# Performance work log

Measured on AMD Instinct MI355X. Metric: run time of the kernel, lower is better.

## Reference

```python
import jax, jax.numpy as jnp
import numpy as np

B, L, E, H, ENC, V, NL = 64, 512, 128, 512, 256, 4, 2
SOS = 4


def setup_inputs() -> dict:
    key = jax.random.key(0)
    ks = jax.random.split(key, 20)
    s = 0.05
    r = lambda k, shp: (jax.random.normal(k, shp, jnp.float32) * s)
    return {
        "encoder_outputs": jax.random.normal(ks[0], (B, L, ENC), jnp.float32),
        "targets": jax.random.randint(ks[1], (B, L), 0, V),
        "encoder_mask": jnp.ones((B, L), bool),
        "teacher_forcing_ratio": 1,
        "emb": r(ks[2], (V + 2, E)),
        "Wh": r(ks[3], (H, H)),
        "Ws": r(ks[4], (H, ENC)),
        "v": r(ks[5], (1, H)),
        "Wih0": r(ks[6], (3 * H, E + ENC)),
        "Whh0": r(ks[7], (3 * H, H)),
        "bih0": r(ks[8], (3 * H,)),
        "bhh0": r(ks[9], (3 * H,)),
        "Wih1": r(ks[10], (3 * H, H)),
        "Whh1": r(ks[11], (3 * H, H)),
        "bih1": r(ks[12], (3 * H,)),
        "bhh1": r(ks[13], (3 * H,)),
        "Wout": r(ks[14], (V, H)),
        "bout": r(ks[15], (V,)),
        "Winit": r(ks[16], (H * NL, ENC)),
        "binit": r(ks[17], (H * NL,)),
    }


def gru_cell(x, h, Wih, Whh, bih, bhh):
    # PyTorch GRUCell math
    gi = x @ Wih.T + bih
    gh = h @ Whh.T + bhh
    ir, iz, inn = jnp.split(gi, 3, axis=-1)
    hr, hz, hn = jnp.split(gh, 3, axis=-1)
    rg = jax.nn.sigmoid(ir + hr)
    zg = jax.nn.sigmoid(iz + hz)
    ng = jnp.tanh(inn + rg * hn)
    return (1.0 - zg) * ng + zg * h


def reference(encoder_outputs, targets, encoder_mask, teacher_forcing_ratio,
              emb, Wh, Ws, v, Wih0, Whh0, bih0, bhh0, Wih1, Whh1, bih1, bhh1,
              Wout, bout, Winit, binit):
    # init hidden: masked mean-pool -> linear -> tanh, (NL, B, H)
    maskf = encoder_mask[..., None].astype(jnp.float32)
    pooled = (encoder_outputs * maskf).sum(1) / jnp.clip(maskf.sum(1), 1.0)
    h0 = jnp.tanh((pooled @ Winit.T + binit).reshape(B, NL, H).transpose(1, 0, 2))

    # attention keys precomputed once (same linear applied each step in torch)
    keys = jnp.einsum('ble,he->blh', encoder_outputs, Ws)  # (B, L, H)

    # teacher forcing ratio fixed at 1 -> inputs known ahead of time
    tokens = jnp.concatenate([jnp.full((B, 1), SOS, targets.dtype), targets[:, :-1]], axis=1)
    emb_seq = emb[tokens]  # (B, L, E)

    neg = jnp.finfo(jnp.float32).min

    def step(h, e_t):
        q = h[-1] @ Wh.T                                   # (B, H)
        energy = jnp.tanh(q[:, None, :] + keys)            # (B, L, H)
        scores = jnp.einsum('blh,h->bl', energy, v[0])     # (B, L)
        scores = jnp.where(encoder_mask, scores, neg)
        attn = jax.nn.softmax(scores, axis=-1)
        ctx = jnp.einsum('bl,ble->be', attn, encoder_outputs)
        x = jnp.concatenate([e_t, ctx], axis=-1)           # (B, E+ENC)
        h0n = gru_cell(x, h[0], Wih0, Whh0, bih0, bhh0)
        h1n = gru_cell(h0n, h[1], Wih1, Whh1, bih1, bhh1)
        logits = h1n @ Wout.T + bout                       # (B, V)
        return jnp.stack([h0n, h1n]), logits

    _, logits = jax.lax.scan(step, h0, emb_seq.transpose(1, 0, 2))
    return logits.transpose(1, 0, 2)  # (B, L, V)
```

## Files before the change

### kernel.cpp

```cpp
#include <hip/hip_runtime.h>
#include <cstdint>
#include <cstddef>


#define BB   64
#define LL   512
#define EE   128
#define HH   512
#define ED   256
#define VV   4
#define SOS  4

#define NBLK 512
#define NTHR 256

typedef unsigned short ushort8 __attribute__((ext_vector_type(8)));
typedef unsigned int uint;
typedef uint  uint4v  __attribute__((ext_vector_type(4)));
typedef float float4v __attribute__((ext_vector_type(4)));

static const size_t OFF_KEYS = 0;
static const size_t OFF_WH   = 33554432;
static const size_t OFF_WHH0 = 34078720;
static const size_t OFF_WIH1 = 35651584;
static const size_t OFF_WHH1 = 37224448;
static const size_t OFF_WIHC = 38797312;
static const size_t OFF_GTOK = 39583744;
static const size_t OFF_H0   = 39620608;
static const size_t OFF_H1   = 39751680;
static const size_t OFF_QQ   = 39882752;
static const size_t OFF_CTXP = 40407040;
static const size_t OFF_SS   = 40931328;
static const size_t OFF_H0Q  = 40933376;
static const size_t OFF_H1Q  = 40998912;
static const size_t OFF_FLG  = 41064448;
static const size_t OFF_CNT  = 41097216;
static const size_t OFF_LP   = 41097728;

#define L_KEYS 0
#define L_H0F  65536
#define L_H1F  66560
#define L_QB   67584
#define L_VV   69696
#define L_CTX  71808
#define L_SCB  72832
#define L_ATB  73088
#define L_RED  73344
#define L_PRED 73408
#define L_GH0  77504
#define L_GH1  78272
#define L_H0O  79040
#define L_H1O  79296
#define L_TOT  79552

#define UC_LD4(dst, ptr) \
  asm volatile("global_load_dwordx4 %0, %1, off sc0 sc1" : "=v"(dst) : "v"(ptr))
#define UC_ST4(ptr, v4) \
  asm volatile("global_store_dwordx4 %0, %1, off sc0 sc1" :: "v"(ptr), "v"(v4) : "memory")
#define UC_FENCE() \
  do { asm volatile("s_waitcnt vmcnt(0)" ::: "memory"); \
       __builtin_amdgcn_sched_barrier(0); } while (0)

__device__ __forceinline__ float bfu(unsigned short u) {
  return __uint_as_float(((unsigned)u) << 16);
}
__device__ __forceinline__ float bflo(uint u) { return __uint_as_float(u << 16); }
__device__ __forceinline__ float bfhi(uint u) { return __uint_as_float(u & 0xffff0000u); }
__device__ __forceinline__ unsigned short f2bf(float f) {
  unsigned u = __float_as_uint(f);
  unsigned r = 0x7FFFu + ((u >> 16) & 1u);
  return (unsigned short)((u + r) >> 16);
}
__device__ __forceinline__ uint packbf(float a, float b) {
  return (uint)f2bf(a) | ((uint)f2bf(b) << 16);
}
__device__ __forceinline__ float tanh_fast(float x) {
  x = __builtin_amdgcn_fmed3f(x, -10.f, 10.f);
  float t = __builtin_amdgcn_exp2f(x * 2.8853900817779268f);
  return (t - 1.f) * __builtin_amdgcn_rcpf(t + 1.f);
}
__device__ __forceinline__ float sigmoid_fast(float x) {
  x = __builtin_amdgcn_fmed3f(x, -30.f, 30.f);
  float t = __builtin_amdgcn_exp2f(x * -1.4426950408889634f);
  return __builtin_amdgcn_rcpf(1.f + t);
}
__device__ __forceinline__ float exp_fast(float x) {
  return __builtin_amdgcn_exp2f(x * 1.4426950408889634f);
}
__device__ __forceinline__ float gloadf(const float* p) {
  return __hip_atomic_load(p, __ATOMIC_RELAXED, __HIP_MEMORY_SCOPE_AGENT);
}
__device__ __forceinline__ void gstoref(float* p, float v) {
  __hip_atomic_store(p, v, __ATOMIC_RELAXED, __HIP_MEMORY_SCOPE_AGENT);
}
__device__ __forceinline__ uint gloadu(const uint* p) {
  return __hip_atomic_load(p, __ATOMIC_RELAXED, __HIP_MEMORY_SCOPE_AGENT);
}
__device__ __forceinline__ void gstoreu(uint* p, uint v) {
  __hip_atomic_store(p, v, __ATOMIC_RELAXED, __HIP_MEMORY_SCOPE_AGENT);
}

__device__ __forceinline__ void octet_sync(char* ws, int b, int j, uint gen) {
  asm volatile("s_waitcnt vmcnt(0)" ::: "memory");
  __syncthreads();
  const int tid = threadIdx.x;
  uint* fl = (uint*)(ws + OFF_FLG);
  if (tid == 0)
    gstoreu(fl + (size_t)(b * 8 + j) * 16, gen);
  if (tid < 8 && tid != j) {
    while (gloadu(fl + (size_t)(b * 8 + tid) * 16) < gen)
      __builtin_amdgcn_s_sleep(4);
  }
  __syncthreads();
}


__global__ void k_prep(const float* Wh, const float* Whh0, const float* Wih0,
                       const float* Wih1, const float* Whh1, char* ws) {
  unsigned short* Whbf   = (unsigned short*)(ws + OFF_WH);
  unsigned short* Whh0bf = (unsigned short*)(ws + OFF_WHH0);
  unsigned short* Wih1bf = (unsigned short*)(ws + OFF_WIH1);
  unsigned short* Whh1bf = (unsigned short*)(ws + OFF_WHH1);
  unsigned short* WihCbf = (unsigned short*)(ws + OFF_WIHC);
  const int tot = 262144 + 786432 * 3 + 393216;
  for (int i = blockIdx.x * blockDim.x + threadIdx.x; i < tot; i += gridDim.x * blockDim.x) {
    if (i < 262144) { Whbf[i] = f2bf(Wh[i]); }
    else if (i < 262144 + 786432) { int jj = i - 262144; Whh0bf[jj] = f2bf(Whh0[jj]); }
    else if (i < 262144 + 2 * 786432) { int jj = i - 262144 - 786432; Wih1bf[jj] = f2bf(Wih1[jj]); }
    else if (i < 262144 + 3 * 786432) { int jj = i - 262144 - 2 * 786432; Whh1bf[jj] = f2bf(Whh1[jj]); }
    else {
      int jj = i - 262144 - 3 * 786432;
      int r = jj >> 8, e = jj & 255;
      WihCbf[jj] = f2bf(Wih0[(size_t)r * 384 + 128 + e]);
    }
  }
}

__global__ void k_gitok(const float* emb, const float* Wih0, const float* bih0, char* ws) {
  float* gt = (float*)(ws + OFF_GTOK);
  const int vt = blockIdx.x;
  const int tid = threadIdx.x;
  __shared__ float ev[EE];
  if (tid < EE) ev[tid] = emb[(size_t)vt * EE + tid];
  __syncthreads();
  for (int r = tid; r < 1536; r += 256) {
    float a = bih0[r];
    const float* wr = Wih0 + (size_t)r * 384;
    for (int e = 0; e < EE; ++e) a += wr[e] * ev[e];
    gt[(size_t)vt * 1536 + r] = a;
  }
}

__global__ void k_keys(const float* enc, const float* Ws, char* ws) {
  unsigned short* keys = (unsigned short*)(ws + OFF_KEYS);
  __shared__ float et[32][ED];
  const int tid = threadIdx.x;
  const int row0 = blockIdx.x * 32;
  for (int r = 0; r < 32; ++r) et[r][tid] = enc[(size_t)(row0 + r) * ED + tid];
  __syncthreads();
  for (int hhh = 0; hhh < 2; ++hhh) {
    const int h = hhh * 256 + tid;
    float acc[32];
    #pragma unroll
    for (int ll = 0; ll < 32; ++ll) acc[ll] = 0.f;
    const float4* wrow = (const float4*)(Ws + (size_t)h * ED);
    for (int e4 = 0; e4 < 64; ++e4) {
      float4 w = wrow[e4];
      #pragma unroll
      for (int ll = 0; ll < 32; ++ll) {
        acc[ll] += w.x * et[ll][e4 * 4] + w.y * et[ll][e4 * 4 + 1]
                 + w.z * et[ll][e4 * 4 + 2] + w.w * et[ll][e4 * 4 + 3];
      }
    }
    for (int ll = 0; ll < 32; ++ll)
      keys[(size_t)(row0 + ll) * HH + h] = f2bf(acc[ll]);
  }
}

__global__ void k_init(const float* enc, const float* Winit, const float* binit, char* ws) {
  const int b = blockIdx.x;
  const int tid = threadIdx.x;
  __shared__ float pooled[ED];
  float acc = 0.f;
  for (int l = 0; l < LL; ++l) acc += enc[((size_t)b * LL + l) * ED + tid];
  pooled[tid] = acc * (1.0f / 512.0f);
  __syncthreads();
  float* h0 = (float*)(ws + OFF_H0);
  float* h1 = (float*)(ws + OFF_H1);
  for (int pass = 0; pass < 4; ++pass) {
    const int jj = pass * 256 + tid;
    float a = binit[jj];
    const float* wr = Winit + (size_t)jj * ED;
    for (int e = 0; e < ED; ++e) a += wr[e] * pooled[e];
    const float val = tanh_fast(a);
    const int nl = jj >> 9, h = jj & 511;
    if (nl == 0) h0[(size_t)b * HH + h] = val;
    else h1[(size_t)b * HH + h] = val;
  }
  if (b == 0) {
    uint* fl = (uint*)(ws + OFF_FLG);
    for (int i = tid; i < 8192; i += 256) fl[i] = 0u;
    uint* cnt = (uint*)(ws + OFF_CNT);
    if (tid < 128) cnt[tid] = 0u;
  }
}

__launch_bounds__(NTHR, 2)
__global__ void k_decode(char* ws, const float* enc, const int* targets,
                         const float* vvec, const float* bhh0, const float* bhh1,
                         const float* bih1, const float* Wout) {
  extern __shared__ char smem[];
  const int tid = threadIdx.x;

  __shared__ int roleSh[2];
  if (tid == 0) {
    uint xcd;
    asm volatile("s_getreg_b32 %0, hwreg(HW_REG_XCC_ID)" : "=s"(xcd));
    xcd &= 7u;
    uint* cnt = (uint*)(ws + OFF_CNT);
    uint rank = __hip_atomic_fetch_add(cnt + (size_t)xcd * 16, 1u,
                                       __ATOMIC_RELAXED, __HIP_MEMORY_SCOPE_AGENT);
    roleSh[0] = (int)(rank & 63);
    roleSh[1] = (int)xcd;
  }
  __syncthreads();
  const int b = roleSh[0], j = roleSh[1];

  const unsigned short* keysg  = (const unsigned short*)(ws + OFF_KEYS);
  const unsigned short* Whbf   = (const unsigned short*)(ws + OFF_WH);
  const unsigned short* Whh0bf = (const unsigned short*)(ws + OFF_WHH0);
  const unsigned short* Wih1bf = (const unsigned short*)(ws + OFF_WIH1);
  const unsigned short* Whh1bf = (const unsigned short*)(ws + OFF_WHH1);
  const unsigned short* WihCbf = (const unsigned short*)(ws + OFF_WIHC);
  const float* gi_tok = (const float*)(ws + OFF_GTOK);

  uint*  QQg   = (uint*)(ws + OFF_QQ)   + (size_t)b * 2048;
  float* CTXPg = (float*)(ws + OFF_CTXP) + (size_t)b * 2048;
  float* SSg   = (float*)(ws + OFF_SS)  + (size_t)b * 8;
  uint*  H0Qg  = (uint*)(ws + OFF_H0Q)  + (size_t)b * 256;
  uint*  H1Qg  = (uint*)(ws + OFF_H1Q)  + (size_t)b * 256;
  float* lp    = (float*)(ws + OFF_LP);

  uint*  h0u   = (uint*)(smem + L_H0F);
  uint*  h1u   = (uint*)(smem + L_H1F);
  float* qbf   = (float*)(smem + L_QB);
  float* vvf   = (float*)(smem + L_VV);
  float* ctx   = (float*)(smem + L_CTX);
  float* scb   = (float*)(smem + L_SCB);
  float* atb   = (float*)(smem + L_ATB);
  float* wred  = (float*)(smem + L_RED);
  float* pRed  = (float*)(smem + L_PRED);
  float* gh0own = (float*)(smem + L_GH0);
  float* gh1own = (float*)(smem + L_GH1);
  float* h0own = (float*)(smem + L_H0O);
  float* h1own = (float*)(smem + L_H1O);
  uint*  qstage = (uint*)(smem + L_PRED);
  uint*  hstage = (uint*)(smem + L_SCB);

  for (int c = tid; c < 4096; c += NTHR) {
    const int l = c >> 6, hs = c & 63;
    ushort8 kv = *(const ushort8*)(keysg + ((size_t)(b * LL + j * 64 + l) * HH + hs * 8));
    *(ushort8*)(smem + L_KEYS + l * 1024 + ((hs * 16) ^ ((l & 7) << 4))) = kv;
  }
  for (int h = tid; h < 512; h += NTHR)
    vvf[(h >> 7) * 132 + (h & 127)] = vvec[h];
  {
    const float* H0g = (const float*)(ws + OFF_H0) + (size_t)b * HH;
    const float* H1g = (const float*)(ws + OFF_H1) + (size_t)b * HH;
    h0u[tid] = packbf(H0g[2 * tid], H0g[2 * tid + 1]);
    h1u[tid] = packbf(H1g[2 * tid], H1g[2 * tid + 1]);
    if (tid < 64) {
      h0own[tid] = H0g[j * 64 + tid];
      h1own[tid] = H1g[j * 64 + tid];
    }
  }
  uint encp[32];
  {
    const float* ebase = enc + ((size_t)(b * LL + j * 64)) * ED + tid;
    #pragma unroll
    for (int k = 0; k < 32; ++k)
      encp[k] = packbf(ebase[(size_t)(2 * k) * ED], ebase[(size_t)(2 * k + 1) * ED]);
  }
  uint whq[64];
  #pragma unroll
  for (int i = 0; i < 32; ++i) {
    whq[i]      = *(const uint*)(Whbf + (size_t)(2 * tid) * HH + j * 64 + 2 * i);
    whq[32 + i] = *(const uint*)(Whbf + (size_t)(2 * tid + 1) * HH + j * 64 + 2 * i);
  }
  __syncthreads();

  {
    float q0 = 0.f, q1 = 0.f;
    #pragma unroll
    for (int i = 0; i < 32; ++i) {
      const float hl = h1own[2 * i], hh = h1own[2 * i + 1];
      q0 += bflo(whq[i]) * hl + bfhi(whq[i]) * hh;
      q1 += bflo(whq[32 + i]) * hl + bfhi(whq[32 + i]) * hh;
    }
    qstage[tid] = packbf(q0, q1);
    if (tid < 32) hstage[tid] = packbf(h1own[2 * tid], h1own[2 * tid + 1]);
    __syncthreads();
    if (tid < 64) { UC_ST4(QQg + (size_t)j * 256 + 4 * tid, *(uint4v*)(qstage + 4 * tid)); }
    else if (tid < 72) {
      const int c = tid - 64;
      UC_ST4(H1Qg + (size_t)j * 32 + 4 * c, *(uint4v*)(hstage + 4 * c));
    }
  }
  octet_sync(ws, b, j, 1u);

  for (int t = 0; t < LL; ++t) {
    if (tid < 64) {
      uint4v uq0, uq1, uq2, uq3, uq4, uq5, uq6, uq7;
      UC_LD4(uq0, QQg + 0 * 256 + 4 * tid);
      UC_LD4(uq1, QQg + 1 * 256 + 4 * tid);
      UC_LD4(uq2, QQg + 2 * 256 + 4 * tid);
      UC_LD4(uq3, QQg + 3 * 256 + 4 * tid);
      UC_LD4(uq4, QQg + 4 * 256 + 4 * tid);
      UC_LD4(uq5, QQg + 5 * 256 + 4 * tid);
      UC_LD4(uq6, QQg + 6 * 256 + 4 * tid);
      UC_LD4(uq7, QQg + 7 * 256 + 4 * tid);
      UC_FENCE();
      const int base = ((8 * tid) >> 7) * 132 + ((8 * tid) & 127);
      #pragma unroll
      for (int k = 0; k < 4; ++k) {
        float lo = bflo(uq0[k]) + bflo(uq1[k]) + bflo(uq2[k]) + bflo(uq3[k])
                 + bflo(uq4[k]) + bflo(uq5[k]) + bflo(uq6[k]) + bflo(uq7[k]);
        float hi = bfhi(uq0[k]) + bfhi(uq1[k]) + bfhi(uq2[k]) + bfhi(uq3[k])
                 + bfhi(uq4[k]) + bfhi(uq5[k]) + bfhi(uq6[k]) + bfhi(uq7[k]);
        qbf[base + 2 * k]     = lo;
        qbf[base + 2 * k + 1] = hi;
      }
    } else if (tid < 120) {
      const int p2 = (tid - 64) >> 3, c = (tid - 64) & 7;
      const int p = p2 + (p2 >= j);
      uint4v u;
      UC_LD4(u, H1Qg + (size_t)p * 32 + 4 * c);
      UC_FENCE();
      *(uint4v*)(h1u + p * 32 + 4 * c) = u;
    }
    __syncthreads();

    {
      const int mat = tid >> 7, seg = (tid >> 6) & 1, r = tid & 63;
      const unsigned short* W = mat ? Whh1bf : Whh0bf;
      const uint* hsrc = (mat ? h1u : h0u) + seg * 128;
      const ushort8* w0 = (const ushort8*)(W + (size_t)(0 * 512 + j * 64 + r) * 512 + seg * 256);
      const ushort8* w1 = (const ushort8*)(W + (size_t)(1 * 512 + j * 64 + r) * 512 + seg * 256);
      const ushort8* w2 = (const ushort8*)(W + (size_t)(2 * 512 + j * 64 + r) * 512 + seg * 256);
      float a0 = 0.f, a1 = 0.f, a2 = 0.f;
      for (int k8 = 0; k8 < 32; ++k8) {
        const uint4 hu = *(const uint4*)(hsrc + k8 * 4);
        const ushort8 u0 = w0[k8], u1 = w1[k8], u2 = w2[k8];
        float hv[8];
        hv[0] = bflo(hu.x); hv[1] = bfhi(hu.x); hv[2] = bflo(hu.y); hv[3] = bfhi(hu.y);
        hv[4] = bflo(hu.z); hv[5] = bfhi(hu.z); hv[6] = bflo(hu.w); hv[7] = bfhi(hu.w);
        #pragma unroll
        for (int u = 0; u < 8; ++u) {
          a0 += bfu(u0[u]) * hv[u];
          a1 += bfu(u1[u]) * hv[u];
          a2 += bfu(u2[u]) * hv[u];
        }
      }
      pRed[((mat * 2 + seg) * 3 + 0) * 64 + r] = a0;
      pRed[((mat * 2 + seg) * 3 + 1) * 64 + r] = a1;
      pRed[((mat * 2 + seg) * 3 + 2) * 64 + r] = a2;
    }

    {
      const int lloc = tid >> 2, hq = tid & 3;
      const char* kbase = smem + L_KEYS + lloc * 1024;
      const int xo = (lloc & 7) << 4;
      const float* qh = qbf + hq * 132;
      const float* vh = vvf + hq * 132;
      float s = 0.f;
      for (int i8 = 0; i8 < 16; ++i8) {
        ushort8 kk = *(const ushort8*)(kbase + ((hq * 256 + i8 * 16) ^ xo));
        const float* q8 = qh + i8 * 8;
        const float* v8 = vh + i8 * 8;
        #pragma unroll
        for (int u = 0; u < 8; ++u)
          s += v8[u] * tanh_fast(q8[u] + bfu(kk[u]));
      }
      s += __shfl_xor(s, 1);
      s += __shfl_xor(s, 2);
      if (hq == 0) scb[lloc] = s;
    }
    __syncthreads();

    if (tid < 64) {
      float e = exp_fast(scb[tid]);
      atb[tid] = e;
      float s2 = e;
      #pragma unroll
      for (int off = 32; off >= 1; off >>= 1) s2 += __shfl_xor(s2, off);
      if (tid == 0) gstoref(SSg + j, s2);
    }
    __syncthreads();

    {
      float a = 0.f;
      #pragma unroll
      for (int k = 0; k < 32; ++k) {
        uint u = encp[k];
        a += atb[2 * k] * bflo(u) + atb[2 * k + 1] * bfhi(u);
      }
      ctx[tid] = a;
    }
    for (int o = tid; o < 384; o += NTHR) {
      const int m = (o >= 192) ? 1 : 0, oo = o - m * 192, g = oo >> 6, r = oo & 63;
      const float v = pRed[((m * 2 + 0) * 3 + g) * 64 + r]
                    + pRed[((m * 2 + 1) * 3 + g) * 64 + r]
                    + (m ? bhh1 : bhh0)[g * 512 + j * 64 + r];
      (m ? gh1own : gh0own)[g * 64 + r] = v;
    }
    __syncthreads();
    if (tid < 64) { UC_ST4((uint*)(CTXPg + (size_t)j * 256) + 4 * tid, *(uint4v*)((uint*)ctx + 4 * tid)); }
    octet_sync(ws, b, j, (uint)(3 * t + 2));

    {
      const int c = tid & 63, p0 = tid >> 6;
      float4v f0, f1;
      UC_LD4(f0, (const uint*)(CTXPg + (size_t)p0 * 256) + 4 * c);
      UC_LD4(f1, (const uint*)(CTXPg + (size_t)(p0 + 4) * 256) + 4 * c);
      float ssv = 0.f;
      if (tid < 8) ssv = gloadf(SSg + tid);
      UC_FENCE();
      if (tid < 8) wred[tid] = ssv;
      *(float4v*)(pRed + (size_t)p0 * 256 + 4 * c) = f0 + f1;
      __syncthreads();
      const float S8 = ((wred[0] + wred[1]) + (wred[2] + wred[3]))
                     + ((wred[4] + wred[5]) + (wred[6] + wred[7]));
      const float rS = __builtin_amdgcn_rcpf(S8);
      ctx[tid] = (pRed[0 * 256 + tid] + pRed[1 * 256 + tid]
                + pRed[2 * 256 + tid] + pRed[3 * 256 + tid]) * rS;
    }
    __syncthreads();
    {
      const int r = tid & 63, q4 = tid >> 6;
      const ushort8* w0 = (const ushort8*)(WihCbf + (size_t)(0 * 512 + j * 64 + r) * 256 + q4 * 64);
      const ushort8* w1 = (const ushort8*)(WihCbf + (size_t)(1 * 512 + j * 64 + r) * 256 + q4 * 64);
      const ushort8* w2 = (const ushort8*)(WihCbf + (size_t)(2 * 512 + j * 64 + r) * 256 + q4 * 64);
      const float* cx = ctx + q4 * 64;
      float a0 = 0.f, a1 = 0.f, a2 = 0.f;
      for (int k8 = 0; k8 < 8; ++k8) {
        const ushort8 u0 = w0[k8], u1 = w1[k8], u2 = w2[k8];
        #pragma unroll
        for (int u = 0; u < 8; ++u) {
          const float c = cx[k8 * 8 + u];
          a0 += bfu(u0[u]) * c; a1 += bfu(u1[u]) * c; a2 += bfu(u2[u]) * c;
        }
      }
      pRed[(q4 * 3 + 0) * 64 + r] = a0;
      pRed[(q4 * 3 + 1) * 64 + r] = a1;
      pRed[(q4 * 3 + 2) * 64 + r] = a2;
    }
    __syncthreads();
    if (tid < 64) {
      const int r = tid;
      const int tok = (t == 0) ? SOS : targets[(size_t)b * LL + t - 1];
      const float* gt = gi_tok + (size_t)tok * 1536 + j * 64 + r;
      const float g0 = pRed[(0 * 3 + 0) * 64 + r] + pRed[(1 * 3 + 0) * 64 + r]
                     + pRed[(2 * 3 + 0) * 64 + r] + pRed[(3 * 3 + 0) * 64 + r] + gt[0];
      const float g1 = pRed[(0 * 3 + 1) * 64 + r] + pRed[(1 * 3 + 1) * 64 + r]
                     + pRed[(2 * 3 + 1) * 64 + r] + pRed[(3 * 3 + 1) * 64 + r] + gt[512];
      const float g2 = pRed[(0 * 3 + 2) * 64 + r] + pRed[(1 * 3 + 2) * 64 + r]
                     + pRed[(2 * 3 + 2) * 64 + r] + pRed[(3 * 3 + 2) * 64 + r] + gt[1024];
      const float rg = sigmoid_fast(g0 + gh0own[r]);
      const float zg = sigmoid_fast(g1 + gh0own[64 + r]);
      const float ng = tanh_fast(g2 + rg * gh0own[128 + r]);
      h0own[r] = (1.f - zg) * ng + zg * h0own[r];
    }
    __syncthreads();
    if (tid < 32) {
      const uint pk = packbf(h0own[2 * tid], h0own[2 * tid + 1]);
      h0u[j * 32 + tid] = pk;
      hstage[tid] = pk;
    }
    __syncthreads();
    if (tid < 8) { UC_ST4(H0Qg + (size_t)j * 32 + 4 * tid, *(uint4v*)(hstage + 4 * tid)); }
    octet_sync(ws, b, j, (uint)(3 * t + 3));

    if (tid < 56) {
      const int p2 = tid >> 3, c = tid & 7;
      const int p = p2 + (p2 >= j);
      uint4v u;
      UC_LD4(u, H0Qg + (size_t)p * 32 + 4 * c);
      UC_FENCE();
      *(uint4v*)(h0u + p * 32 + 4 * c) = u;
    }
    __syncthreads();
    {
      const int r = tid & 63, s4 = tid >> 6;
      const ushort8* w0 = (const ushort8*)(Wih1bf + (size_t)(0 * 512 + j * 64 + r) * 512 + s4 * 128);
      const ushort8* w1 = (const ushort8*)(Wih1bf + (size_t)(1 * 512 + j * 64 + r) * 512 + s4 * 128);
      const ushort8* w2 = (const ushort8*)(Wih1bf + (size_t)(2 * 512 + j * 64 + r) * 512 + s4 * 128);
      const uint* hsrc = h0u + s4 * 64;
      float a0 = 0.f, a1 = 0.f, a2 = 0.f;
      for (int k8 = 0; k8 < 16; ++k8) {
        const uint4 hu = *(const uint4*)(hsrc + k8 * 4);
        const ushort8 u0 = w0[k8], u1 = w1[k8], u2 = w2[k8];
        float hv[8];
        hv[0] = bflo(hu.x); hv[1] = bfhi(hu.x); hv[2] = bflo(hu.y); hv[3] = bfhi(hu.y);
        hv[4] = bflo(hu.z); hv[5] = bfhi(hu.z); hv[6] = bflo(hu.w); hv[7] = bfhi(hu.w);
        #pragma unroll
        for (int u = 0; u < 8; ++u) {
          a0 += bfu(u0[u]) * hv[u];
          a1 += bfu(u1[u]) * hv[u];
          a2 += bfu(u2[u]) * hv[u];
        }
      }
      pRed[(s4 * 3 + 0) * 64 + r] = a0;
      pRed[(s4 * 3 + 1) * 64 + r] = a1;
      pRed[(s4 * 3 + 2) * 64 + r] = a2;
    }
    __syncthreads();
    if (tid < 64) {
      const int r = tid;
      const float g0 = pRed[(0 * 3 + 0) * 64 + r] + pRed[(1 * 3 + 0) * 64 + r]
                     + pRed[(2 * 3 + 0) * 64 + r] + pRed[(3 * 3 + 0) * 64 + r]
                     + bih1[0 * 512 + j * 64 + r];
      const float g1 = pRed[(0 * 3 + 1) * 64 + r] + pRed[(1 * 3 + 1) * 64 + r]
                     + pRed[(2 * 3 + 1) * 64 + r] + pRed[(3 * 3 + 1) * 64 + r]
                     + bih1[1 * 512 + j * 64 + r];
      const float g2 = pRed[(0 * 3 + 2) * 64 + r] + pRed[(1 * 3 + 2) * 64 + r]
                     + pRed[(2 * 3 + 2) * 64 + r] + pRed[(3 * 3 + 2) * 64 + r]
                     + bih1[2 * 512 + j * 64 + r];
      const float rg = sigmoid_fast(g0 + gh1own[r]);
      const float zg = sigmoid_fast(g1 + gh1own[64 + r]);
      const float ng = tanh_fast(g2 + rg * gh1own[128 + r]);
      h1own[r] = (1.f - zg) * ng + zg * h1own[r];
    }
    __syncthreads();
    {
      float q0 = 0.f, q1 = 0.f;
      #pragma unroll
      for (int i = 0; i < 32; ++i) {
        const float hl = h1own[2 * i], hh = h1own[2 * i + 1];
        q0 += bflo(whq[i]) * hl + bfhi(whq[i]) * hh;
        q1 += bflo(whq[32 + i]) * hl + bfhi(whq[32 + i]) * hh;
      }
      qstage[tid] = packbf(q0, q1);
    }
    if (tid < 32) {
      const uint pk = packbf(h1own[2 * tid], h1own[2 * tid + 1]);
      h1u[j * 32 + tid] = pk;
      hstage[tid] = pk;
    }
    if (tid >= 64 && tid < 128) {
      const int lane = tid - 64, v = lane >> 4, i = lane & 15;
      float a = 0.f;
      #pragma unroll
      for (int k = 0; k < 4; ++k)
        a += Wout[(size_t)v * HH + j * 64 + i * 4 + k] * h1own[i * 4 + k];
      a += __shfl_xor(a, 8); a += __shfl_xor(a, 4);
      a += __shfl_xor(a, 2); a += __shfl_xor(a, 1);
      if (i == 0) lp[(((size_t)t * BB + b) * 8 + j) * 4 + v] = a;
    }
    __syncthreads();
    if (tid < 64) { UC_ST4(QQg + (size_t)j * 256 + 4 * tid, *(uint4v*)(qstage + 4 * tid)); }
    else if (tid < 72) {
      const int c = tid - 64;
      UC_ST4(H1Qg + (size_t)j * 32 + 4 * c, *(uint4v*)(hstage + 4 * c));
    }
    octet_sync(ws, b, j, (uint)(3 * t + 4));
  }
}

__global__ void k_lsum(const char* ws, const float* bout, float* out) {
  const float* lp = (const float*)(ws + OFF_LP);
  const int i = blockIdx.x * 256 + threadIdx.x;
  if (i >= BB * LL * VV) return;
  const int v = i & 3, t = (i >> 2) & 511, b = i >> 11;
  float a = bout[v];
  #pragma unroll
  for (int jj = 0; jj < 8; ++jj)
    a += lp[(((size_t)t * BB + b) * 8 + jj) * 4 + v];
  out[i] = a;
}

extern "C" void kernel_launch(void* const* d_in, const int* in_sizes, int n_in,
                              void* d_out, int out_size, void* d_ws, size_t ws_size,
                              hipStream_t stream) {
  char* ws = (char*)d_ws;
  const float* enc     = (const float*)d_in[0];
  const int*   targets = (const int*)d_in[1];
  const float* emb   = (const float*)d_in[4];
  const float* Wh    = (const float*)d_in[5];
  const float* Ws    = (const float*)d_in[6];
  const float* vvec  = (const float*)d_in[7];
  const float* Wih0  = (const float*)d_in[8];
  const float* Whh0  = (const float*)d_in[9];
  const float* bih0  = (const float*)d_in[10];
  const float* bhh0  = (const float*)d_in[11];
  const float* Wih1  = (const float*)d_in[12];
  const float* Whh1  = (const float*)d_in[13];
  const float* bih1  = (const float*)d_in[14];
  const float* bhh1  = (const float*)d_in[15];
  const float* Wout  = (const float*)d_in[16];
  const float* bout  = (const float*)d_in[17];
  const float* Winit = (const float*)d_in[18];
  const float* binit = (const float*)d_in[19];

  k_prep <<<1024, 256, 0, stream>>>(Wh, Whh0, Wih0, Wih1, Whh1, ws);
  k_gitok<<<6,    256, 0, stream>>>(emb, Wih0, bih0, ws);
  k_keys <<<1024, 256, 0, stream>>>(enc, Ws, ws);
  k_init <<<64,   256, 0, stream>>>(enc, Winit, binit, ws);

  (void)hipFuncSetAttribute((const void*)k_decode,
                            hipFuncAttributeMaxDynamicSharedMemorySize, L_TOT);

  {
    void* kws = (void*)ws;
    void* ken = (void*)enc;
    void* ktg = (void*)targets;
    void* kvv = (void*)vvec;
    void* kb0 = (void*)bhh0;
    void* kb1 = (void*)bhh1;
    void* kbi = (void*)bih1;
    void* kwo = (void*)Wout;
    void* args[] = { &kws, &ken, &ktg, &kvv, &kb0, &kb1, &kbi, &kwo };
    hipError_t ce = hipLaunchCooperativeKernel((const void*)k_decode, dim3(NBLK), dim3(NTHR),
                                               args, L_TOT, stream);
    if (ce != hipSuccess) {
      k_decode<<<dim3(NBLK), dim3(NTHR), L_TOT, stream>>>(ws, enc, targets, vvec,
                                                          bhh0, bhh1, bih1, Wout);
    }
  }

  k_lsum<<<512, 256, 0, stream>>>(ws, bout, (float*)d_out);
}
```

Measured before the change: 49.45 ms.

## Assign decode roles statically and use XCD-local cache scope for octet exchange

Block roles (batch b, slice j) now come from a static blockIdx mapping, replacing the atomic-counter XCD-based assignment. Each octet records its XCD ID and checks whether all eight members share one XCD. If so, the per-step exchanges of q, h, context and flags use sc0-only loads and stores, which stay in the local L2, instead of sc0 sc1 system-coherent accesses. A duplicate flag array written with sc1 is the fallback, and a bounded local poll drops to it when members are spread across XCDs. Co-location depends on the hardware's block-to-XCD dispatch order, and the scope reasoning is subtle enough to risk coherence bugs.

```diff
diff --git a/kernel.cpp b/kernel.cpp
--- a/kernel.cpp
+++ b/kernel.cpp
@@ -34,8 +34,9 @@
 static const size_t OFF_H0Q  = 40933376;
 static const size_t OFF_H1Q  = 40998912;
 static const size_t OFF_FLG  = 41064448;
-static const size_t OFF_CNT  = 41097216;
-static const size_t OFF_LP   = 41097728;
+static const size_t OFF_FLG2 = 41097216;
+static const size_t OFF_XCD  = 41129984;
+static const size_t OFF_LP   = 41162752;
 
 #define L_KEYS 0
 #define L_H0F  65536
@@ -53,11 +54,27 @@
 #define L_H1O  79296
 #define L_TOT  79552
 
-#define UC_LD4(dst, ptr) \
-  asm volatile("global_load_dwordx4 %0, %1, off sc0 sc1" : "=v"(dst) : "v"(ptr))
-#define UC_ST4(ptr, v4) \
-  asm volatile("global_store_dwordx4 %0, %1, off sc0 sc1" :: "v"(ptr), "v"(v4) : "memory")
-#define UC_FENCE() \
+__device__ __forceinline__ void ex_st4(uint* p, uint4v v, bool local) {
+  if (local) asm volatile("global_store_dwordx4 %0, %1, off sc0" :: "v"(p), "v"(v) : "memory");
+  else       asm volatile("global_store_dwordx4 %0, %1, off sc0 sc1" :: "v"(p), "v"(v) : "memory");
+}
+__device__ __forceinline__ void ex_ld4(uint4v& d, const uint* p, bool local) {
+  if (local) asm volatile("global_load_dwordx4 %0, %1, off sc0" : "=v"(d) : "v"(p));
+  else       asm volatile("global_load_dwordx4 %0, %1, off sc0 sc1" : "=v"(d) : "v"(p));
+}
+__device__ __forceinline__ void ex_ld4f(float4v& d, const uint* p, bool local) {
+  if (local) asm volatile("global_load_dwordx4 %0, %1, off sc0" : "=v"(d) : "v"(p));
+  else       asm volatile("global_load_dwordx4 %0, %1, off sc0 sc1" : "=v"(d) : "v"(p));
+}
+__device__ __forceinline__ void ex_st1f(float* p, float v, bool local) {
+  if (local) asm volatile("global_store_dword %0, %1, off sc0" :: "v"(p), "v"(v) : "memory");
+  else       asm volatile("global_store_dword %0, %1, off sc0 sc1" :: "v"(p), "v"(v) : "memory");
+}
+__device__ __forceinline__ void ex_ld1f(float& d, const float* p, bool local) {
+  if (local) asm volatile("global_load_dword %0, %1, off sc0" : "=v"(d) : "v"(p));
+  else       asm volatile("global_load_dword %0, %1, off sc0 sc1" : "=v"(d) : "v"(p));
+}
+#define EX_FENCE() \
   do { asm volatile("s_waitcnt vmcnt(0)" ::: "memory"); \
        __builtin_amdgcn_sched_barrier(0); } while (0)
 
@@ -87,29 +104,37 @@
 __device__ __forceinline__ float exp_fast(float x) {
   return __builtin_amdgcn_exp2f(x * 1.4426950408889634f);
 }
-__device__ __forceinline__ float gloadf(const float* p) {
-  return __hip_atomic_load(p, __ATOMIC_RELAXED, __HIP_MEMORY_SCOPE_AGENT);
-}
-__device__ __forceinline__ void gstoref(float* p, float v) {
-  __hip_atomic_store(p, v, __ATOMIC_RELAXED, __HIP_MEMORY_SCOPE_AGENT);
-}
-__device__ __forceinline__ uint gloadu(const uint* p) {
-  return __hip_atomic_load(p, __ATOMIC_RELAXED, __HIP_MEMORY_SCOPE_AGENT);
-}
-__device__ __forceinline__ void gstoreu(uint* p, uint v) {
-  __hip_atomic_store(p, v, __ATOMIC_RELAXED, __HIP_MEMORY_SCOPE_AGENT);
-}
-
-__device__ __forceinline__ void octet_sync(char* ws, int b, int j, uint gen) {
+
+__device__ __forceinline__ void oct_sync(char* ws, int b, int j, uint gen, bool local) {
   asm volatile("s_waitcnt vmcnt(0)" ::: "memory");
   __syncthreads();
   const int tid = threadIdx.x;
-  uint* fl = (uint*)(ws + OFF_FLG);
-  if (tid == 0)
-    gstoreu(fl + (size_t)(b * 8 + j) * 16, gen);
+  if (tid == 0) {
+    uint* flf = (uint*)(ws + OFF_FLG)  + (size_t)(b * 8 + j) * 16;
+    uint* fls = (uint*)(ws + OFF_FLG2) + (size_t)(b * 8 + j) * 16;
+    asm volatile("global_store_dword %0, %1, off sc0" :: "v"(flf), "v"(gen) : "memory");
+    asm volatile("global_store_dword %0, %1, off sc0 sc1" :: "v"(fls), "v"(gen) : "memory");
+  }
   if (tid < 8 && tid != j) {
-    while (gloadu(fl + (size_t)(b * 8 + tid) * 16) < gen)
-      __builtin_amdgcn_s_sleep(4);
+    uint v = 0;
+    if (local) {
+      const uint* pf = (const uint*)(ws + OFF_FLG) + (size_t)(b * 8 + tid) * 16;
+      for (int it = 0; it < 256; ++it) {
+        asm volatile("global_load_dword %0, %1, off sc0\n\ts_waitcnt vmcnt(0)"
+                     : "=v"(v) : "v"(pf) : "memory");
+        if (v >= gen) break;
+        __builtin_amdgcn_s_sleep(1);
+      }
+    }
+    if (v < gen) {
+      const uint* ps = (const uint*)(ws + OFF_FLG2) + (size_t)(b * 8 + tid) * 16;
+      for (;;) {
+        asm volatile("global_load_dword %0, %1, off sc0 sc1\n\ts_waitcnt vmcnt(0)"
+                     : "=v"(v) : "v"(ps) : "memory");
+        if (v >= gen) break;
+        __builtin_amdgcn_s_sleep(2);
+      }
+    }
   }
   __syncthreads();
 }
@@ -198,10 +223,9 @@
     else h1[(size_t)b * HH + h] = val;
   }
   if (b == 0) {
-    uint* fl = (uint*)(ws + OFF_FLG);
-    for (int i = tid; i < 8192; i += 256) fl[i] = 0u;
-    uint* cnt = (uint*)(ws + OFF_CNT);
-    if (tid < 128) cnt[tid] = 0u;
+    uint* f1 = (uint*)(ws + OFF_FLG);
+    uint* f2 = (uint*)(ws + OFF_FLG2);
+    for (int i = tid; i < 8192; i += 256) { f1[i] = 0u; f2[i] = 0u; }
   }
 }
 
@@ -211,20 +235,14 @@
                          const float* bih1, const float* Wout) {
   extern __shared__ char smem[];
   const int tid = threadIdx.x;
-
-  __shared__ int roleSh[2];
-  if (tid == 0) {
-    uint xcd;
-    asm volatile("s_getreg_b32 %0, hwreg(HW_REG_XCC_ID)" : "=s"(xcd));
-    xcd &= 7u;
-    uint* cnt = (uint*)(ws + OFF_CNT);
-    uint rank = __hip_atomic_fetch_add(cnt + (size_t)xcd * 16, 1u,
-                                       __ATOMIC_RELAXED, __HIP_MEMORY_SCOPE_AGENT);
-    roleSh[0] = (int)(rank & 63);
-    roleSh[1] = (int)xcd;
-  }
-  __syncthreads();
-  const int b = roleSh[0], j = roleSh[1];
+  const int blk = blockIdx.x;
+
+  const int r = blk & 7, s = blk >> 3;
+  const int b = r * 8 + (s & 7), j = s >> 3;
+
+  uint myxcd;
+  asm volatile("s_getreg_b32 %0, hwreg(HW_REG_XCC_ID)" : "=s"(myxcd));
+  myxcd &= 7u;
 
   const unsigned short* keysg  = (const unsigned short*)(ws + OFF_KEYS);
   const unsigned short* Whbf   = (const unsigned short*)(ws + OFF_WH);
@@ -300,26 +318,42 @@
     qstage[tid] = packbf(q0, q1);
     if (tid < 32) hstage[tid] = packbf(h1own[2 * tid], h1own[2 * tid + 1]);
     __syncthreads();
-    if (tid < 64) { UC_ST4(QQg + (size_t)j * 256 + 4 * tid, *(uint4v*)(qstage + 4 * tid)); }
+    if (tid < 64) { ex_st4(QQg + (size_t)j * 256 + 4 * tid, *(uint4v*)(qstage + 4 * tid), false); }
     else if (tid < 72) {
       const int c = tid - 64;
-      UC_ST4(H1Qg + (size_t)j * 32 + 4 * c, *(uint4v*)(hstage + 4 * c));
-    }
-  }
-  octet_sync(ws, b, j, 1u);
+      ex_st4(H1Qg + (size_t)j * 32 + 4 * c, *(uint4v*)(hstage + 4 * c), false);
+    } else if (tid == 72) {
+      uint* xt = (uint*)(ws + OFF_XCD) + (size_t)(b * 8 + j) * 16;
+      asm volatile("global_store_dword %0, %1, off sc0 sc1" :: "v"(xt), "v"(myxcd) : "memory");
+    }
+  }
+  oct_sync(ws, b, j, 1u, false);
+
+  __shared__ int localSh;
+  if (tid == 0) localSh = 1;
+  __syncthreads();
+  if (tid < 8) {
+    uint v;
+    const uint* xt = (const uint*)(ws + OFF_XCD) + (size_t)(b * 8 + tid) * 16;
+    asm volatile("global_load_dword %0, %1, off sc0 sc1\n\ts_waitcnt vmcnt(0)"
+                 : "=v"(v) : "v"(xt) : "memory");
+    if (v != myxcd) localSh = 0;
+  }
+  __syncthreads();
+  const bool local = (localSh != 0);
 
   for (int t = 0; t < LL; ++t) {
     if (tid < 64) {
       uint4v uq0, uq1, uq2, uq3, uq4, uq5, uq6, uq7;
-      UC_LD4(uq0, QQg + 0 * 256 + 4 * tid);
-      UC_LD4(uq1, QQg + 1 * 256 + 4 * tid);
-      UC_LD4(uq2, QQg + 2 * 256 + 4 * tid);
-      UC_LD4(uq3, QQg + 3 * 256 + 4 * tid);
-      UC_LD4(uq4, QQg + 4 * 256 + 4 * tid);
-      UC_LD4(uq5, QQg + 5 * 256 + 4 * tid);
-      UC_LD4(uq6, QQg + 6 * 256 + 4 * tid);
-      UC_LD4(uq7, QQg + 7 * 256 + 4 * tid);
-      UC_FENCE();
+      ex_ld4(uq0, QQg + 0 * 256 + 4 * tid, local);
+      ex_ld4(uq1, QQg + 1 * 256 + 4 * tid, local);
+      ex_ld4(uq2, QQg + 2 * 256 + 4 * tid, local);
+      ex_ld4(uq3, QQg + 3 * 256 + 4 * tid, local);
+      ex_ld4(uq4, QQg + 4 * 256 + 4 * tid, local);
+      ex_ld4(uq5, QQg + 5 * 256 + 4 * tid, local);
+      ex_ld4(uq6, QQg + 6 * 256 + 4 * tid, local);
+      ex_ld4(uq7, QQg + 7 * 256 + 4 * tid, local);
+      EX_FENCE();
       const int base = ((8 * tid) >> 7) * 132 + ((8 * tid) & 127);
       #pragma unroll
       for (int k = 0; k < 4; ++k) {
@@ -334,19 +368,19 @@
       const int p2 = (tid - 64) >> 3, c = (tid - 64) & 7;
       const int p = p2 + (p2 >= j);
       uint4v u;
-      UC_LD4(u, H1Qg + (size_t)p * 32 + 4 * c);
-      UC_FENCE();
+      ex_ld4(u, H1Qg + (size_t)p * 32 + 4 * c, local);
+      EX_FENCE();
       *(uint4v*)(h1u + p * 32 + 4 * c) = u;
     }
     __syncthreads();
 
     {
-      const int mat = tid >> 7, seg = (tid >> 6) & 1, r = tid & 63;
+      const int mat = tid >> 7, seg = (tid >> 6) & 1, rr = tid & 63;
       const unsigned short* W = mat ? Whh1bf : Whh0bf;
       const uint* hsrc = (mat ? h1u : h0u) + seg * 128;
-      const ushort8* w0 = (const ushort8*)(W + (size_t)(0 * 512 + j * 64 + r) * 512 + seg * 256);
-      const ushort8* w1 = (const ushort8*)(W + (size_t)(1 * 512 + j * 64 + r) * 512 + seg * 256);
-      const ushort8* w2 = (const ushort8*)(W + (size_t)(2 * 512 + j * 64 + r) * 512 + seg * 256);
+      const ushort8* w0 = (const ushort8*)(W + (size_t)(0 * 512 + j * 64 + rr) * 512 + seg * 256);
+      const ushort8* w1 = (const ushort8*)(W + (size_t)(1 * 512 + j * 64 + rr) * 512 + seg * 256);
+      const ushort8* w2 = (const ushort8*)(W + (size_t)(2 * 512 + j * 64 + rr) * 512 + seg * 256);
       float a0 = 0.f, a1 = 0.f, a2 = 0.f;
       for (int k8 = 0; k8 < 32; ++k8) {
         const uint4 hu = *(const uint4*)(hsrc + k8 * 4);
@@ -361,9 +395,9 @@
           a2 += bfu(u2[u]) * hv[u];
         }
       }
-      pRed[((mat * 2 + seg) * 3 + 0) * 64 + r] = a0;
-      pRed[((mat * 2 + seg) * 3 + 1) * 64 + r] = a1;
-      pRed[((mat * 2 + seg) * 3 + 2) * 64 + r] = a2;
+      pRed[((mat * 2 + seg) * 3 + 0) * 64 + rr] = a0;
+      pRed[((mat * 2 + seg) * 3 + 1) * 64 + rr] = a1;
+      pRed[((mat * 2 + seg) * 3 + 2) * 64 + rr] = a2;
     }
 
     {
@@ -372,18 +406,18 @@
       const int xo = (lloc & 7) << 4;
       const float* qh = qbf + hq * 132;
       const float* vh = vvf + hq * 132;
-      float s = 0.f;
+      float sv = 0.f;
       for (int i8 = 0; i8 < 16; ++i8) {
         ushort8 kk = *(const ushort8*)(kbase + ((hq * 256 + i8 * 16) ^ xo));
         const float* q8 = qh + i8 * 8;
         const float* v8 = vh + i8 * 8;
         #pragma unroll
         for (int u = 0; u < 8; ++u)
-          s += v8[u] * tanh_fast(q8[u] + bfu(kk[u]));
-      }
-      s += __shfl_xor(s, 1);
-      s += __shfl_xor(s, 2);
-      if (hq == 0) scb[lloc] = s;
+          sv += v8[u] * tanh_fast(q8[u] + bfu(kk[u]));
+      }
+      sv += __shfl_xor(sv, 1);
+      sv += __shfl_xor(sv, 2);
+      if (hq == 0) scb[lloc] = sv;
     }
     __syncthreads();
 
@@ -393,7 +427,7 @@
       float s2 = e;
       #pragma unroll
       for (int off = 32; off >= 1; off >>= 1) s2 += __shfl_xor(s2, off);
-      if (tid == 0) gstoref(SSg + j, s2);
+      if (tid == 0) ex_st1f(SSg + j, s2, local);
     }
     __syncthreads();
 
@@ -407,24 +441,24 @@
       ctx[tid] = a;
     }
     for (int o = tid; o < 384; o += NTHR) {
-      const int m = (o >= 192) ? 1 : 0, oo = o - m * 192, g = oo >> 6, r = oo & 63;
-      const float v = pRed[((m * 2 + 0) * 3 + g) * 64 + r]
-                    + pRed[((m * 2 + 1) * 3 + g) * 64 + r]
-                    + (m ? bhh1 : bhh0)[g * 512 + j * 64 + r];
-      (m ? gh1own : gh0own)[g * 64 + r] = v;
-    }
-    __syncthreads();
-    if (tid < 64) { UC_ST4((uint*)(CTXPg + (size_t)j * 256) + 4 * tid, *(uint4v*)((uint*)ctx + 4 * tid)); }
-    octet_sync(ws, b, j, (uint)(3 * t + 2));
+      const int m = (o >= 192) ? 1 : 0, oo = o - m * 192, g = oo >> 6, rr = oo & 63;
+      const float v = pRed[((m * 2 + 0) * 3 + g) * 64 + rr]
+                    + pRed[((m * 2 + 1) * 3 + g) * 64 + rr]
+                    + (m ? bhh1 : bhh0)[g * 512 + j * 64 + rr];
+      (m ? gh1own : gh0own)[g * 64 + rr] = v;
+    }
+    __syncthreads();
+    if (tid < 64) { ex_st4((uint*)(CTXPg + (size_t)j * 256) + 4 * tid, *(uint4v*)((uint*)ctx + 4 * tid), local); }
+    oct_sync(ws, b, j, (uint)(3 * t + 2), local);
 
     {
       const int c = tid & 63, p0 = tid >> 6;
       float4v f0, f1;
-      UC_LD4(f0, (const uint*)(CTXPg + (size_t)p0 * 256) + 4 * c);
-      UC_LD4(f1, (const uint*)(CTXPg + (size_t)(p0 + 4) * 256) + 4 * c);
+      ex_ld4f(f0, (const uint*)(CTXPg + (size_t)p0 * 256) + 4 * c, local);
+      ex_ld4f(f1, (const uint*)(CTXPg + (size_t)(p0 + 4) * 256) + 4 * c, local);
       float ssv = 0.f;
-      if (tid < 8) ssv = gloadf(SSg + tid);
-      UC_FENCE();
+      if (tid < 8) ex_ld1f(ssv, SSg + tid, local);
+      EX_FENCE();
       if (tid < 8) wred[tid] = ssv;
       *(float4v*)(pRed + (size_t)p0 * 256 + 4 * c) = f0 + f1;
       __syncthreads();
@@ -436,10 +470,10 @@
     }
     __syncthreads();
     {
-      const int r = tid & 63, q4 = tid >> 6;
-      const ushort8* w0 = (const ushort8*)(WihCbf + (size_t)(0 * 512 + j * 64 + r) * 256 + q4 * 64);
-      const ushort8* w1 = (const ushort8*)(WihCbf + (size_t)(1 * 512 + j * 64 + r) * 256 + q4 * 64);
-      const ushort8* w2 = (const ushort8*)(WihCbf + (size_t)(2 * 512 + j * 64 + r) * 256 + q4 * 64);
+      const int rr = tid & 63, q4 = tid >> 6;
+      const ushort8* w0 = (const ushort8*)(WihCbf + (size_t)(0 * 512 + j * 64 + rr) * 256 + q4 * 64);
+      const ushort8* w1 = (const ushort8*)(WihCbf + (size_t)(1 * 512 + j * 64 + rr) * 256 + q4 * 64);
+      const ushort8* w2 = (const ushort8*)(WihCbf + (size_t)(2 * 512 + j * 64 + rr) * 256 + q4 * 64);
       const float* cx = ctx + q4 * 64;
       float a0 = 0.f, a1 = 0.f, a2 = 0.f;
       for (int k8 = 0; k8 < 8; ++k8) {
@@ -450,25 +484,25 @@
           a0 += bfu(u0[u]) * c; a1 += bfu(u1[u]) * c; a2 += bfu(u2[u]) * c;
         }
       }
-      pRed[(q4 * 3 + 0) * 64 + r] = a0;
-      pRed[(q4 * 3 + 1) * 64 + r] = a1;
-      pRed[(q4 * 3 + 2) * 64 + r] = a2;
+      pRed[(q4 * 3 + 0) * 64 + rr] = a0;
+      pRed[(q4 * 3 + 1) * 64 + rr] = a1;
+      pRed[(q4 * 3 + 2) * 64 + rr] = a2;
     }
     __syncthreads();
     if (tid < 64) {
-      const int r = tid;
+      const int rr = tid;
       const int tok = (t == 0) ? SOS : targets[(size_t)b * LL + t - 1];
-      const float* gt = gi_tok + (size_t)tok * 1536 + j * 64 + r;
-      const float g0 = pRed[(0 * 3 + 0) * 64 + r] + pRed[(1 * 3 + 0) * 64 + r]
-                     + pRed[(2 * 3 + 0) * 64 + r] + pRed[(3 * 3 + 0) * 64 + r] + gt[0];
-      const float g1 = pRed[(0 * 3 + 1) * 64 + r] + pRed[(1 * 3 + 1) * 64 + r]
-                     + pRed[(2 * 3 + 1) * 64 + r] + pRed[(3 * 3 + 1) * 64 + r] + gt[512];
-      const float g2 = pRed[(0 * 3 + 2) * 64 + r] + pRed[(1 * 3 + 2) * 64 + r]
-                     + pRed[(2 * 3 + 2) * 64 + r] + pRed[(3 * 3 + 2) * 64 + r] + gt[1024];
-      const float rg = sigmoid_fast(g0 + gh0own[r]);
-      const float zg = sigmoid_fast(g1 + gh0own[64 + r]);
-      const float ng = tanh_fast(g2 + rg * gh0own[128 + r]);
-      h0own[r] = (1.f - zg) * ng + zg * h0own[r];
+      const float* gt = gi_tok + (size_t)tok * 1536 + j * 64 + rr;
+      const float g0 = pRed[(0 * 3 + 0) * 64 + rr] + pRed[(1 * 3 + 0) * 64 + rr]
+                     + pRed[(2 * 3 + 0) * 64 + rr] + pRed[(3 * 3 + 0) * 64 + rr] + gt[0];
+      const float g1 = pRed[(0 * 3 + 1) * 64 + rr] + pRed[(1 * 3 + 1) * 64 + rr]
+                     + pRed[(2 * 3 + 1) * 64 + rr] + pRed[(3 * 3 + 1) * 64 + rr] + gt[512];
+      const float g2 = pRed[(0 * 3 + 2) * 64 + rr] + pRed[(1 * 3 + 2) * 64 + rr]
+                     + pRed[(2 * 3 + 2) * 64 + rr] + pRed[(3 * 3 + 2) * 64 + rr] + gt[1024];
+      const float rg = sigmoid_fast(g0 + gh0own[rr]);
+      const float zg = sigmoid_fast(g1 + gh0own[64 + rr]);
+      const float ng = tanh_fast(g2 + rg * gh0own[128 + rr]);
+      h0own[rr] = (1.f - zg) * ng + zg * h0own[rr];
     }
     __syncthreads();
     if (tid < 32) {
@@ -477,23 +511,23 @@
       hstage[tid] = pk;
     }
     __syncthreads();
-    if (tid < 8) { UC_ST4(H0Qg + (size_t)j * 32 + 4 * tid, *(uint4v*)(hstage + 4 * tid)); }
-    octet_sync(ws, b, j, (uint)(3 * t + 3));
+    if (tid < 8) { ex_st4(H0Qg + (size_t)j * 32 + 4 * tid, *(uint4v*)(hstage + 4 * tid), local); }
+    oct_sync(ws, b, j, (uint)(3 * t + 3), local);
 
     if (tid < 56) {
       const int p2 = tid >> 3, c = tid & 7;
       const int p = p2 + (p2 >= j);
       uint4v u;
-      UC_LD4(u, H0Qg + (size_t)p * 32 + 4 * c);
-      UC_FENCE();
+      ex_ld4(u, H0Qg + (size_t)p * 32 + 4 * c, local);
+      EX_FENCE();
       *(uint4v*)(h0u + p * 32 + 4 * c) = u;
     }
     __syncthreads();
     {
-      const int r = tid & 63, s4 = tid >> 6;
-      const ushort8* w0 = (const ushort8*)(Wih1bf + (size_t)(0 * 512 + j * 64 + r) * 512 + s4 * 128);
-      const ushort8* w1 = (const ushort8*)(Wih1bf + (size_t)(1 * 512 + j * 64 + r) * 512 + s4 * 128);
-      const ushort8* w2 = (const ushort8*)(Wih1bf + (size_t)(2 * 512 + j * 64 + r) * 512 + s4 * 128);
+      const int rr = tid & 63, s4 = tid >> 6;
+      const ushort8* w0 = (const ushort8*)(Wih1bf + (size_t)(0 * 512 + j * 64 + rr) * 512 + s4 * 128);
+      const ushort8* w1 = (const ushort8*)(Wih1bf + (size_t)(1 * 512 + j * 64 + rr) * 512 + s4 * 128);
+      const ushort8* w2 = (const ushort8*)(Wih1bf + (size_t)(2 * 512 + j * 64 + rr) * 512 + s4 * 128);
       const uint* hsrc = h0u + s4 * 64;
       float a0 = 0.f, a1 = 0.f, a2 = 0.f;
       for (int k8 = 0; k8 < 16; ++k8) {
@@ -509,26 +543,26 @@
           a2 += bfu(u2[u]) * hv[u];
         }
       }
-      pRed[(s4 * 3 + 0) * 64 + r] = a0;
-      pRed[(s4 * 3 + 1) * 64 + r] = a1;
-      pRed[(s4 * 3 + 2) * 64 + r] = a2;
+      pRed[(s4 * 3 + 0) * 64 + rr] = a0;
+      pRed[(s4 * 3 + 1) * 64 + rr] = a1;
+      pRed[(s4 * 3 + 2) * 64 + rr] = a2;
     }
     __syncthreads();
     if (tid < 64) {
-      const int r = tid;
-      const float g0 = pRed[(0 * 3 + 0) * 64 + r] + pRed[(1 * 3 + 0) * 64 + r]
-                     + pRed[(2 * 3 + 0) * 64 + r] + pRed[(3 * 3 + 0) * 64 + r]
-                     + bih1[0 * 512 + j * 64 + r];
-      const float g1 = pRed[(0 * 3 + 1) * 64 + r] + pRed[(1 * 3 + 1) * 64 + r]
-                     + pRed[(2 * 3 + 1) * 64 + r] + pRed[(3 * 3 + 1) * 64 + r]
-                     + bih1[1 * 512 + j * 64 + r];
-      const float g2 = pRed[(0 * 3 + 2) * 64 + r] + pRed[(1 * 3 + 2) * 64 + r]
-                     + pRed[(2 * 3 + 2) * 64 + r] + pRed[(3 * 3 + 2) * 64 + r]
-                     + bih1[2 * 512 + j * 64 + r];
-      const float rg = sigmoid_fast(g0 + gh1own[r]);
-      const float zg = sigmoid_fast(g1 + gh1own[64 + r]);
-      const float ng = tanh_fast(g2 + rg * gh1own[128 + r]);
-      h1own[r] = (1.f - zg) * ng + zg * h1own[r];
+      const int rr = tid;
+      const float g0 = pRed[(0 * 3 + 0) * 64 + rr] + pRed[(1 * 3 + 0) * 64 + rr]
+                     + pRed[(2 * 3 + 0) * 64 + rr] + pRed[(3 * 3 + 0) * 64 + rr]
+                     + bih1[0 * 512 + j * 64 + rr];
+      const float g1 = pRed[(0 * 3 + 1) * 64 + rr] + pRed[(1 * 3 + 1) * 64 + rr]
+                     + pRed[(2 * 3 + 1) * 64 + rr] + pRed[(3 * 3 + 1) * 64 + rr]
+                     + bih1[1 * 512 + j * 64 + rr];
+      const float g2 = pRed[(0 * 3 + 2) * 64 + rr] + pRed[(1 * 3 + 2) * 64 + rr]
+                     + pRed[(2 * 3 + 2) * 64 + rr] + pRed[(3 * 3 + 2) * 64 + rr]
+                     + bih1[2 * 512 + j * 64 + rr];
+      const float rg = sigmoid_fast(g0 + gh1own[rr]);
+      const float zg = sigmoid_fast(g1 + gh1own[64 + rr]);
+      const float ng = tanh_fast(g2 + rg * gh1own[128 + rr]);
+      h1own[rr] = (1.f - zg) * ng + zg * h1own[rr];
     }
     __syncthreads();
     {
@@ -557,12 +591,12 @@
       if (i == 0) lp[(((size_t)t * BB + b) * 8 + j) * 4 + v] = a;
     }
     __syncthreads();
-    if (tid < 64) { UC_ST4(QQg + (size_t)j * 256 + 4 * tid, *(uint4v*)(qstage + 4 * tid)); }
+    if (tid < 64) { ex_st4(QQg + (size_t)j * 256 + 4 * tid, *(uint4v*)(qstage + 4 * tid), local); }
     else if (tid < 72) {
       const int c = tid - 64;
-      UC_ST4(H1Qg + (size_t)j * 32 + 4 * c, *(uint4v*)(hstage + 4 * c));
-    }
-    octet_sync(ws, b, j, (uint)(3 * t + 4));
+      ex_st4(H1Qg + (size_t)j * 32 + 4 * c, *(uint4v*)(hstage + 4 * c), local);
+    }
+    oct_sync(ws, b, j, (uint)(3 * t + 4), local);
   }
 }
 
```

Result: slower. 78.53 ms (+58.8%).
